# Optimization experiments

Hardware: AMD Instinct MI355X
Metric: run time of the kernel (lower is better)

The kernel has to match this reference:

```python
import jax, jax.numpy as jnp
import numpy as np

B = 1048576  # batch
A = 3        # number of actors in the ensemble


def _linear_params(key, out_d, in_d):
    """Stacked-over-actors torch.nn.Linear-style init: U(-1/sqrt(in), 1/sqrt(in))."""
    k1, k2 = jax.random.split(key)
    s = 1.0 / np.sqrt(in_d)
    W = jax.random.uniform(k1, (A, out_d, in_d), minval=-s, maxval=s, dtype=jnp.float32)
    b = jax.random.uniform(k2, (A, out_d), minval=-s, maxval=s, dtype=jnp.float32)
    return W, b


def setup_inputs() -> dict:
    key = jax.random.key(0)
    ks = jax.random.split(key, 10)
    spatial = jax.random.normal(ks[0], (B, 3, 9), dtype=jnp.float32)
    car_stats = jax.random.normal(ks[1], (B, 4), dtype=jnp.float32)  # unused by the model
    Wmx, bmx = _linear_params(ks[2], 10, 6)
    Wnx, bnx = _linear_params(ks[3], 10, 3)
    Wmy, bmy = _linear_params(ks[4], 10, 6)
    Wny, bny = _linear_params(ks[5], 10, 3)
    Wmz, bmz = _linear_params(ks[6], 5, 6)
    Wnz, bnz = _linear_params(ks[7], 5, 3)
    Wlin, blin = _linear_params(ks[8], 25, 25)
    Wout, bout = _linear_params(ks[9], 15, 25)
    return {
        "spatial": spatial, "car_stats": car_stats,
        "Wmx": Wmx, "bmx": bmx, "Wnx": Wnx, "bnx": bnx,
        "Wmy": Wmy, "bmy": bmy, "Wny": Wny, "bny": bny,
        "Wmz": Wmz, "bmz": bmz, "Wnz": Wnz, "bnz": bnz,
        "Wlin": Wlin, "blin": blin, "Wout": Wout, "bout": bout,
    }


def reference(spatial, car_stats,
              Wmx, bmx, Wnx, bnx,
              Wmy, bmy, Wny, bny,
              Wmz, bmz, Wnz, bnz,
              Wlin, blin, Wout, bout):
    # SimpleSpatialInput vectorized over the actor axis 'a':
    # (Linear(6->size)(s[:, :6])) * (Linear(3->size)(s[:, 6:9]))
    def proc(s, Wm, bm, Wn, bn):
        m = jnp.einsum('bi,aoi->bao', s[:, :6], Wm) + bm   # [B, A, size]
        n = jnp.einsum('bi,aoi->bao', s[:, 6:9], Wn) + bn  # [B, A, size]
        return m * n

    px = proc(spatial[:, 0], Wmx, bmx, Wnx, bnx)  # [B, A, 10]
    py = proc(spatial[:, 1], Wmy, bmy, Wny, bny)  # [B, A, 10]
    pz = proc(spatial[:, 2], Wmz, bmz, Wnz, bnz)  # [B, A, 5]
    ps = jnp.concatenate([px, py, pz], axis=-1)   # [B, A, 25]

    h = jnp.einsum('bad,aod->bao', ps, Wlin) + blin  # [B, A, 25]
    h = h / (1.0 + jnp.abs(h))                       # Softsign
    out = jnp.einsum('bad,aod->bao', h, Wout) + bout # [B, A, 15]

    result = jnp.transpose(out, (0, 2, 1))           # [B, 15, A] (stack dim=2)
    multiplier = jax.nn.softmax(result[:, 9, :], axis=1)  # [B, A]
    # stack of result[:, i] * multiplier over i=0..8, cumsum over actors,
    # take last -> plain weighted sum over the actor axis.
    return jnp.einsum('boa,ba->bo', result[:, :9, :], multiplier)  # [B, 9]
```

## Files before the change

### kernel.cpp

```cpp
#include <hip/hip_runtime.h>


typedef _Float16 half8   __attribute__((ext_vector_type(8)));
typedef __fp16   fp16x2  __attribute__((ext_vector_type(2)));
typedef float    floatx4 __attribute__((ext_vector_type(4)));

#define NFRAG 21
#define FRAG_HALFS (NFRAG * 512)
#define TPB 8
#define NWAVES 8

__global__ __launch_bounds__(256) void prep_frags(
    const float* __restrict__ Wmx, const float* __restrict__ bmx,
    const float* __restrict__ Wnx, const float* __restrict__ bnx,
    const float* __restrict__ Wmy, const float* __restrict__ bmy,
    const float* __restrict__ Wny, const float* __restrict__ bny,
    const float* __restrict__ Wmz, const float* __restrict__ bmz,
    const float* __restrict__ Wnz, const float* __restrict__ bnz,
    const float* __restrict__ Wlin, const float* __restrict__ blin,
    const float* __restrict__ Wout, const float* __restrict__ bout,
    _Float16* __restrict__ frag)
{
    int i = threadIdx.x + blockIdx.x * blockDim.x;
    if (i >= FRAG_HALFS) return;
    int f = i >> 9, rem = i & 511;
    int lane = rem >> 3, j = rem & 7;
    int q = lane >> 4, m = lane & 15;
    int a = f / 7, idx = f % 7;
    float v = 0.f;
    if (idx < 4) {
        int c = m + ((idx & 1) ? 16 : 0);
        int k = 8 * q + j;
        bool npart = (idx >= 2);
        if (c < 10) {
            if (!npart) { if (k < 6)             v = Wmx[(a*10 + c)*6 + k];
                          else if (k == 27)      v = bmx[a*10 + c]; }
            else        { if (k >= 6 && k < 9)   v = Wnx[(a*10 + c)*3 + (k-6)];
                          else if (k == 27)      v = bnx[a*10 + c]; }
        } else if (c < 20) {
            if (!npart) { if (k >= 9 && k < 15)  v = Wmy[(a*10 + c-10)*6 + (k-9)];
                          else if (k == 27)      v = bmy[a*10 + c-10]; }
            else        { if (k >= 15 && k < 18) v = Wny[(a*10 + c-10)*3 + (k-15)];
                          else if (k == 27)      v = bny[a*10 + c-10]; }
        } else if (c < 25) {
            if (!npart) { if (k >= 18 && k < 24) v = Wmz[(a*5 + c-20)*6 + (k-18)];
                          else if (k == 27)      v = bmz[a*5 + c-20]; }
            else        { if (k >= 24 && k < 27) v = Wnz[(a*5 + c-20)*3 + (k-24)];
                          else if (k == 27)      v = bnz[a*5 + c-20]; }
        }
    } else if (idx < 6) {
        int o  = m + ((idx == 5) ? 16 : 0);
        int kc = 16 * (j >> 2) + 4 * q + (j & 3);
        if (o < 25) {
            if (kc < 25)       v = Wlin[(a*25 + o)*25 + kc];
            else if (kc == 25) v = blin[a*25 + o];
        }
    } else {
        int ko = 16 * (j >> 2) + 4 * q + (j & 3);
        if (m < 10) {
            if (ko < 25)       v = Wout[(a*15 + m)*25 + ko];
            else if (ko == 25) v = bout[a*15 + m];
        }
    }
    frag[(size_t)f * 512 + lane * 8 + j] = (_Float16)v;
}

__global__ __launch_bounds__(512) void actor_mfma(
    const float* __restrict__ spatial,
    const _Float16* __restrict__ frag,
    float* __restrict__ out)
{
    __shared__ _Float16 lds_f[FRAG_HALFS];
    __shared__ float    lds_o[NWAVES * 144];

    const int t = threadIdx.x;
    const int lane = t & 63, w = t >> 6;
    const int q = lane >> 4, e = lane & 15;
    const size_t b0 = (size_t)blockIdx.x * (16 * NWAVES * TPB);

    {
        const float4* gf = (const float4*)frag;
        float4* df = (float4*)lds_f;
        #pragma unroll
        for (int k = 0; k < 3; ++k) {
            int idx = t + k * 512;
            if (idx < 1344) df[idx] = gf[idx];
        }
    }

    const float* sbase = spatial + (b0 + (size_t)(w * 16 + e)) * 27 + 8 * q;
    float vbase[8];
    #pragma unroll
    for (int j = 0; j < 8; ++j) vbase[j] = ((8 * q + j) == 27) ? 1.f : 0.f;

    float* const ldso = lds_o + w * 144;
    const floatx4 z = {0.f, 0.f, 0.f, 0.f};

    __syncthreads();

    int fo = lane;

    auto loadT = [&](float (&dst)[8], int tt) {
        const float* s_ = sbase + (size_t)tt * (16 * NWAVES * 27);
        #pragma unroll
        for (int j = 0; j < 8; ++j) {
            int k = 8 * q + j;
            dst[j] = (k < 27) ? s_[j] : vbase[j];
        }
    };

    auto tileCompute = [&](const float (&cur)[8], int tt) {
        union H8u { half8 v; fp16x2 p[4]; };

        H8u Bs;
        #pragma unroll
        for (int p_ = 0; p_ < 4; ++p_)
            Bs.p[p_] = __builtin_amdgcn_cvt_pkrtz(cur[2*p_], cur[2*p_+1]);

        floatx4 oacc[3];
        #pragma unroll
        for (int a = 0; a < 3; ++a) {
            asm volatile("" : "+v"(fo));
            const half8* fp = (const half8*)lds_f + fo;
            const int fb = a * 7;
            H8u P;
            {
                floatx4 M0 = __builtin_amdgcn_mfma_f32_16x16x32_f16(fp[(fb+0)*64], Bs.v, z, 0,0,0);
                floatx4 N0 = __builtin_amdgcn_mfma_f32_16x16x32_f16(fp[(fb+2)*64], Bs.v, z, 0,0,0);
                P.p[0] = __builtin_amdgcn_cvt_pkrtz(M0[0]*N0[0], M0[1]*N0[1]);
                P.p[1] = __builtin_amdgcn_cvt_pkrtz(M0[2]*N0[2], M0[3]*N0[3]);
            }
            {
                floatx4 M1 = __builtin_amdgcn_mfma_f32_16x16x32_f16(fp[(fb+1)*64], Bs.v, z, 0,0,0);
                floatx4 N1 = __builtin_amdgcn_mfma_f32_16x16x32_f16(fp[(fb+3)*64], Bs.v, z, 0,0,0);
                float g5 = (q == 2) ? 1.f : M1[1]*N1[1];
                P.p[2] = __builtin_amdgcn_cvt_pkrtz(M1[0]*N1[0], g5);
                P.p[3] = __builtin_amdgcn_cvt_pkrtz(M1[2]*N1[2], M1[3]*N1[3]);
            }

            floatx4 H0 = __builtin_amdgcn_mfma_f32_16x16x32_f16(fp[(fb+4)*64], P.v, z, 0,0,0);
            floatx4 H1 = __builtin_amdgcn_mfma_f32_16x16x32_f16(fp[(fb+5)*64], P.v, z, 0,0,0);

            auto ss = [](float v_) {
                return v_ * __builtin_amdgcn_rcpf(1.0f + __builtin_fabsf(v_));
            };
            H8u Hh;
            Hh.p[0] = __builtin_amdgcn_cvt_pkrtz(ss(H0[0]), ss(H0[1]));
            Hh.p[1] = __builtin_amdgcn_cvt_pkrtz(ss(H0[2]), ss(H0[3]));
            float h5 = (q == 2) ? 1.f : ss(H1[1]);
            Hh.p[2] = __builtin_amdgcn_cvt_pkrtz(ss(H1[0]), h5);
            Hh.p[3] = __builtin_amdgcn_cvt_pkrtz(ss(H1[2]), ss(H1[3]));

            oacc[a] = __builtin_amdgcn_mfma_f32_16x16x32_f16(fp[(fb+6)*64], Hh.v, z, 0,0,0);
        }

        const int src9 = 32 + e;
        float g0 = __shfl(oacc[0][1], src9, 64);
        float g1 = __shfl(oacc[1][1], src9, 64);
        float g2 = __shfl(oacc[2][1], src9, 64);
        float mx = fmaxf(g0, fmaxf(g1, g2));
        float e0 = __expf(g0 - mx);
        float e1 = __expf(g1 - mx);
        float e2 = __expf(g2 - mx);
        float inv = __builtin_amdgcn_rcpf(e0 + e1 + e2);
        e0 *= inv; e1 *= inv; e2 *= inv;

        float res[4];
        #pragma unroll
        for (int r = 0; r < 4; ++r)
            res[r] = oacc[0][r] * e0 + oacc[1][r] * e1 + oacc[2][r] * e2;

        if (q < 2) {
            #pragma unroll
            for (int r = 0; r < 4; ++r) ldso[e * 9 + 4 * q + r] = res[r];
        } else if (q == 2) {
            ldso[e * 9 + 8] = res[0];
        }
        if (lane < 36) {
            float4 v = *(const float4*)(ldso + lane * 4);
            *(float4*)(out + (b0 + (size_t)tt * (16 * NWAVES) + w * 16) * 9 + lane * 4) = v;
        }
    };

    float sA[8], sB[8];
    loadT(sA, 0);
    for (int tt = 0; tt < TPB; tt += 2) {
        loadT(sB, tt + 1);
        tileCompute(sA, tt);
        if (tt + 2 < TPB) loadT(sA, tt + 2);
        tileCompute(sB, tt + 1);
    }
}

extern "C" void kernel_launch(void* const* d_in, const int* in_sizes, int n_in,
                              void* d_out, int out_size, void* d_ws, size_t ws_size,
                              hipStream_t stream) {
    const float* spatial = (const float*)d_in[0];
    const float* Wmx  = (const float*)d_in[2];
    const float* bmx  = (const float*)d_in[3];
    const float* Wnx  = (const float*)d_in[4];
    const float* bnx  = (const float*)d_in[5];
    const float* Wmy  = (const float*)d_in[6];
    const float* bmy  = (const float*)d_in[7];
    const float* Wny  = (const float*)d_in[8];
    const float* bny  = (const float*)d_in[9];
    const float* Wmz  = (const float*)d_in[10];
    const float* bmz  = (const float*)d_in[11];
    const float* Wnz  = (const float*)d_in[12];
    const float* bnz  = (const float*)d_in[13];
    const float* Wlin = (const float*)d_in[14];
    const float* blin = (const float*)d_in[15];
    const float* Wout = (const float*)d_in[16];
    const float* bout = (const float*)d_in[17];
    float* out = (float*)d_out;

    _Float16* frag = (_Float16*)d_ws;

    prep_frags<<<dim3(42), dim3(256), 0, stream>>>(
        Wmx, bmx, Wnx, bnx, Wmy, bmy, Wny, bny, Wmz, bmz, Wnz, bnz,
        Wlin, blin, Wout, bout, frag);

    const int nb = in_sizes[0] / 27;
    dim3 grid(nb / (16 * NWAVES * TPB));
    actor_mfma<<<grid, dim3(64 * NWAVES), 0, stream>>>(spatial, frag, out);
}
```

Measured before the change: 227.3 us.

## Split actors across waves with register-resident weights and LDS softmax combine

Each wave now handles a single actor for a 16-row tile instead of looping over all three actors. Its seven weight fragments are held in registers rather than read from LDS for every tile. Per-actor outputs go into a double-buffered LDS area, and after a block barrier one rotating wave per group computes the softmax-weighted sum and writes the result. This trades LDS fragment traffic and serial per-wave work for three-fold redundant spatial loads, a __syncthreads per tile, and a softmax that no longer subtracts the max, which could overflow for large logits.

```diff
diff --git a/kernel.cpp b/kernel.cpp
--- a/kernel.cpp
+++ b/kernel.cpp
@@ -8,7 +8,8 @@
 #define NFRAG 21
 #define FRAG_HALFS (NFRAG * 512)
 #define TPB 8
-#define NWAVES 8
+#define NGROUP 2
+#define NWAVES (NGROUP * 3)
 
 __global__ __launch_bounds__(256) void prep_frags(
     const float* __restrict__ Wmx, const float* __restrict__ bmx,
@@ -65,120 +66,117 @@
     frag[(size_t)f * 512 + lane * 8 + j] = (_Float16)v;
 }
 
-__global__ __launch_bounds__(512) void actor_mfma(
+__global__ __launch_bounds__(64 * NWAVES) void actor_mfma(
     const float* __restrict__ spatial,
     const _Float16* __restrict__ frag,
     float* __restrict__ out)
 {
-    __shared__ _Float16 lds_f[FRAG_HALFS];
-    __shared__ float    lds_o[NWAVES * 144];
+    __shared__ float comb[2][NGROUP * 3 * 16 * 12];
+    __shared__ float lds_o[NGROUP * 144];
 
     const int t = threadIdx.x;
     const int lane = t & 63, w = t >> 6;
+    const int a = w % 3;
+    const int g = w / 3;
     const int q = lane >> 4, e = lane & 15;
-    const size_t b0 = (size_t)blockIdx.x * (16 * NWAVES * TPB);
-
-    {
-        const float4* gf = (const float4*)frag;
-        float4* df = (float4*)lds_f;
-        #pragma unroll
-        for (int k = 0; k < 3; ++k) {
-            int idx = t + k * 512;
-            if (idx < 1344) df[idx] = gf[idx];
-        }
-    }
-
-    const float* sbase = spatial + (b0 + (size_t)(w * 16 + e)) * 27 + 8 * q;
-    float vbase[8];
+    const size_t b0 = (size_t)blockIdx.x * (16 * NGROUP * TPB);
+
+    const _Float16* fbp = frag + (size_t)(a * 7) * 512 + lane * 8;
+    half8 F[7];
     #pragma unroll
-    for (int j = 0; j < 8; ++j) vbase[j] = ((8 * q + j) == 27) ? 1.f : 0.f;
-
-    float* const ldso = lds_o + w * 144;
+    for (int i = 0; i < 7; ++i) F[i] = *(const half8*)(fbp + i * 512);
+    #pragma unroll
+    for (int i = 0; i < 7; ++i) asm volatile("" : "+v"(F[i]));
+
+    const float* sbase = spatial + (b0 + (size_t)(g * 16 + e)) * 27 + 8 * q;
+    float* const ldso = lds_o + g * 144;
     const floatx4 z = {0.f, 0.f, 0.f, 0.f};
 
-    __syncthreads();
-
-    int fo = lane;
+    union H8u { half8 v; fp16x2 p[4]; };
 
     auto loadT = [&](float (&dst)[8], int tt) {
-        const float* s_ = sbase + (size_t)tt * (16 * NWAVES * 27);
+        const float* s_ = sbase + (size_t)tt * (16 * NGROUP * 27);
         #pragma unroll
         for (int j = 0; j < 8; ++j) {
             int k = 8 * q + j;
-            dst[j] = (k < 27) ? s_[j] : vbase[j];
+            float v = (k == 27) ? 1.f : 0.f;
+            if (k < 27) v = s_[j];
+            dst[j] = v;
         }
     };
 
+    auto ss = [](float v_) {
+        return v_ * __builtin_amdgcn_rcpf(1.0f + __builtin_fabsf(v_));
+    };
+
     auto tileCompute = [&](const float (&cur)[8], int tt) {
-        union H8u { half8 v; fp16x2 p[4]; };
-
         H8u Bs;
         #pragma unroll
         for (int p_ = 0; p_ < 4; ++p_)
             Bs.p[p_] = __builtin_amdgcn_cvt_pkrtz(cur[2*p_], cur[2*p_+1]);
 
-        floatx4 oacc[3];
-        #pragma unroll
-        for (int a = 0; a < 3; ++a) {
-            asm volatile("" : "+v"(fo));
-            const half8* fp = (const half8*)lds_f + fo;
-            const int fb = a * 7;
-            H8u P;
-            {
-                floatx4 M0 = __builtin_amdgcn_mfma_f32_16x16x32_f16(fp[(fb+0)*64], Bs.v, z, 0,0,0);
-                floatx4 N0 = __builtin_amdgcn_mfma_f32_16x16x32_f16(fp[(fb+2)*64], Bs.v, z, 0,0,0);
-                P.p[0] = __builtin_amdgcn_cvt_pkrtz(M0[0]*N0[0], M0[1]*N0[1]);
-                P.p[1] = __builtin_amdgcn_cvt_pkrtz(M0[2]*N0[2], M0[3]*N0[3]);
+        H8u P;
+        {
+            floatx4 M0 = __builtin_amdgcn_mfma_f32_16x16x32_f16(F[0], Bs.v, z, 0,0,0);
+            floatx4 N0 = __builtin_amdgcn_mfma_f32_16x16x32_f16(F[2], Bs.v, z, 0,0,0);
+            P.p[0] = __builtin_amdgcn_cvt_pkrtz(M0[0]*N0[0], M0[1]*N0[1]);
+            P.p[1] = __builtin_amdgcn_cvt_pkrtz(M0[2]*N0[2], M0[3]*N0[3]);
+        }
+        {
+            floatx4 M1 = __builtin_amdgcn_mfma_f32_16x16x32_f16(F[1], Bs.v, z, 0,0,0);
+            floatx4 N1 = __builtin_amdgcn_mfma_f32_16x16x32_f16(F[3], Bs.v, z, 0,0,0);
+            float g5 = (q == 2) ? 1.f : M1[1]*N1[1];
+            P.p[2] = __builtin_amdgcn_cvt_pkrtz(M1[0]*N1[0], g5);
+            P.p[3] = __builtin_amdgcn_cvt_pkrtz(M1[2]*N1[2], M1[3]*N1[3]);
+        }
+        floatx4 H0 = __builtin_amdgcn_mfma_f32_16x16x32_f16(F[4], P.v, z, 0,0,0);
+        floatx4 H1 = __builtin_amdgcn_mfma_f32_16x16x32_f16(F[5], P.v, z, 0,0,0);
+        H8u Hh;
+        Hh.p[0] = __builtin_amdgcn_cvt_pkrtz(ss(H0[0]), ss(H0[1]));
+        Hh.p[1] = __builtin_amdgcn_cvt_pkrtz(ss(H0[2]), ss(H0[3]));
+        float h5 = (q == 2) ? 1.f : ss(H1[1]);
+        Hh.p[2] = __builtin_amdgcn_cvt_pkrtz(ss(H1[0]), h5);
+        Hh.p[3] = __builtin_amdgcn_cvt_pkrtz(ss(H1[2]), ss(H1[3]));
+        floatx4 oacc = __builtin_amdgcn_mfma_f32_16x16x32_f16(F[6], Hh.v, z, 0,0,0);
+
+        float* cw_ = &comb[tt & 1][((g * 3 + a) * 16 + e) * 12];
+        if (q < 2) {
+            *(float4*)(cw_ + 4 * q) = *(const float4*)&oacc;
+        } else if (q == 2) {
+            *(float2*)(cw_ + 8) = make_float2(oacc[0], oacc[1]);
+        }
+
+        __syncthreads();
+
+        if (a == tt % 3) {
+            const float* cg = &comb[tt & 1][(g * 3) * 16 * 12];
+            const float* r0 = cg + (e) * 12;
+            const float* r1 = cg + (16 + e) * 12;
+            const float* r2 = cg + (32 + e) * 12;
+            float2 t0 = *(const float2*)(r0 + 8);
+            float2 t1 = *(const float2*)(r1 + 8);
+            float2 t2 = *(const float2*)(r2 + 8);
+            float e0 = __expf(t0.y);
+            float e1 = __expf(t1.y);
+            float e2 = __expf(t2.y);
+            float inv = __builtin_amdgcn_rcpf(e0 + e1 + e2);
+            e0 *= inv; e1 *= inv; e2 *= inv;
+
+            if (q < 2) {
+                float4 v0 = *(const float4*)(r0 + 4 * q);
+                float4 v1 = *(const float4*)(r1 + 4 * q);
+                float4 v2 = *(const float4*)(r2 + 4 * q);
+                ldso[e * 9 + 4 * q + 0] = v0.x * e0 + v1.x * e1 + v2.x * e2;
+                ldso[e * 9 + 4 * q + 1] = v0.y * e0 + v1.y * e1 + v2.y * e2;
+                ldso[e * 9 + 4 * q + 2] = v0.z * e0 + v1.z * e1 + v2.z * e2;
+                ldso[e * 9 + 4 * q + 3] = v0.w * e0 + v1.w * e1 + v2.w * e2;
+            } else if (q == 2) {
+                ldso[e * 9 + 8] = t0.x * e0 + t1.x * e1 + t2.x * e2;
             }
-            {
-                floatx4 M1 = __builtin_amdgcn_mfma_f32_16x16x32_f16(fp[(fb+1)*64], Bs.v, z, 0,0,0);
-                floatx4 N1 = __builtin_amdgcn_mfma_f32_16x16x32_f16(fp[(fb+3)*64], Bs.v, z, 0,0,0);
-                float g5 = (q == 2) ? 1.f : M1[1]*N1[1];
-                P.p[2] = __builtin_amdgcn_cvt_pkrtz(M1[0]*N1[0], g5);
-                P.p[3] = __builtin_amdgcn_cvt_pkrtz(M1[2]*N1[2], M1[3]*N1[3]);
+            if (lane < 36) {
+                float4 v = *(const float4*)(ldso + lane * 4);
+                *(float4*)(out + (b0 + (size_t)tt * (16 * NGROUP) + g * 16) * 9 + lane * 4) = v;
             }
-
-            floatx4 H0 = __builtin_amdgcn_mfma_f32_16x16x32_f16(fp[(fb+4)*64], P.v, z, 0,0,0);
-            floatx4 H1 = __builtin_amdgcn_mfma_f32_16x16x32_f16(fp[(fb+5)*64], P.v, z, 0,0,0);
-
-            auto ss = [](float v_) {
-                return v_ * __builtin_amdgcn_rcpf(1.0f + __builtin_fabsf(v_));
-            };
-            H8u Hh;
-            Hh.p[0] = __builtin_amdgcn_cvt_pkrtz(ss(H0[0]), ss(H0[1]));
-            Hh.p[1] = __builtin_amdgcn_cvt_pkrtz(ss(H0[2]), ss(H0[3]));
-            float h5 = (q == 2) ? 1.f : ss(H1[1]);
-            Hh.p[2] = __builtin_amdgcn_cvt_pkrtz(ss(H1[0]), h5);
-            Hh.p[3] = __builtin_amdgcn_cvt_pkrtz(ss(H1[2]), ss(H1[3]));
-
-            oacc[a] = __builtin_amdgcn_mfma_f32_16x16x32_f16(fp[(fb+6)*64], Hh.v, z, 0,0,0);
-        }
-
-        const int src9 = 32 + e;
-        float g0 = __shfl(oacc[0][1], src9, 64);
-        float g1 = __shfl(oacc[1][1], src9, 64);
-        float g2 = __shfl(oacc[2][1], src9, 64);
-        float mx = fmaxf(g0, fmaxf(g1, g2));
-        float e0 = __expf(g0 - mx);
-        float e1 = __expf(g1 - mx);
-        float e2 = __expf(g2 - mx);
-        float inv = __builtin_amdgcn_rcpf(e0 + e1 + e2);
-        e0 *= inv; e1 *= inv; e2 *= inv;
-
-        float res[4];
-        #pragma unroll
-        for (int r = 0; r < 4; ++r)
-            res[r] = oacc[0][r] * e0 + oacc[1][r] * e1 + oacc[2][r] * e2;
-
-        if (q < 2) {
-            #pragma unroll
-            for (int r = 0; r < 4; ++r) ldso[e * 9 + 4 * q + r] = res[r];
-        } else if (q == 2) {
-            ldso[e * 9 + 8] = res[0];
-        }
-        if (lane < 36) {
-            float4 v = *(const float4*)(ldso + lane * 4);
-            *(float4*)(out + (b0 + (size_t)tt * (16 * NWAVES) + w * 16) * 9 + lane * 4) = v;
         }
     };
 
@@ -221,6 +219,6 @@
         Wlin, blin, Wout, bout, frag);
 
     const int nb = in_sizes[0] / 27;
-    dim3 grid(nb / (16 * NWAVES * TPB));
+    dim3 grid(nb / (16 * NGROUP * TPB));
     actor_mfma<<<grid, dim3(64 * NWAVES), 0, stream>>>(spatial, frag, out);
 }
```

Measured after the change: 266.4 us. 17.2% more time.
